# Kernel tuning notes

Measured on AMD Instinct MI355X. Metric: run time of the kernel, lower is better.

The kernel has to match this reference:

```python
import jax, jax.numpy as jnp
import numpy as np

B, T, D, H = 4, 1024, 2048, 16
E = D // H  # head_dim = 128


def setup_inputs() -> dict:
    key = jax.random.key(0)
    ks = jax.random.split(key, 10)
    s = 1.0 / np.sqrt(D)
    x = jax.random.normal(ks[0], (B, T, D), dtype=jnp.float32)
    attention_mask = jnp.ones((B, T), dtype=jnp.int32)
    # Per-head q/k/v projections stacked along head axis: [H, E, D] weights, [H, E] biases.
    Wq = jax.random.uniform(ks[1], (H, E, D), jnp.float32, -s, s)
    bq = jax.random.uniform(ks[2], (H, E), jnp.float32, -s, s)
    Wk = jax.random.uniform(ks[3], (H, E, D), jnp.float32, -s, s)
    bk = jax.random.uniform(ks[4], (H, E), jnp.float32, -s, s)
    Wv = jax.random.uniform(ks[5], (H, E, D), jnp.float32, -s, s)
    bv = jax.random.uniform(ks[6], (H, E), jnp.float32, -s, s)
    Wo = jax.random.uniform(ks[7], (D, D), jnp.float32, -s, s)
    bo = jax.random.uniform(ks[8], (D,), jnp.float32, -s, s)
    return {"x": x, "attention_mask": attention_mask, "Wq": Wq, "bq": bq,
            "Wk": Wk, "bk": bk, "Wv": Wv, "bv": bv, "Wo": Wo, "bo": bo}


def _causal_mask(Tq, Tk, dtype):
    neg = jnp.finfo(dtype).min
    qi = jnp.arange(Tq)[:, None]
    ki = jnp.arange(Tk)[None, :]
    max_allowed = Tk - Tq + qi
    return jnp.where(ki > max_allowed, neg, jnp.zeros((), dtype)).astype(dtype)


def reference(x, attention_mask, Wq, bq, Wk, bk, Wv, bv, Wo, bo):
    dt = x.dtype
    neg = jnp.finfo(dt).min
    scale = 1.0 / np.sqrt(E)
    # per-head projections (vectorized over heads): [B,H,T,E]
    q = jnp.einsum('btd,hed->bhte', x, Wq) + bq[None, :, None, :]
    k = jnp.einsum('btd,hed->bhte', x, Wk) + bk[None, :, None, :]
    v = jnp.einsum('btd,hed->bhte', x, Wv) + bv[None, :, None, :]
    # scores [B,H,Tq,Tk]
    scores = jnp.einsum('bhqe,bhke->bhqk', q, k) * scale
    scores = scores + _causal_mask(T, T, dt)[None, None]
    keep = attention_mask.astype(bool)  # [B,Tk]
    scores = jnp.where(keep[:, None, None, :], scores, neg)
    probs = jax.nn.softmax(scores, axis=-1)
    y = jnp.einsum('bhqk,bhke->bhqe', probs, v)  # [B,H,T,E]
    # heads concatenated along feature dim in head order
    y = jnp.transpose(y, (0, 2, 1, 3)).reshape(B, T, D)
    out = y @ Wo.T + bo
    return out
```

## Files before the change

### kernel.cpp

```cpp
#include <hip/hip_runtime.h>
#include <hip/hip_bf16.h>


typedef __attribute__((ext_vector_type(4))) float f32x4;
typedef __attribute__((ext_vector_type(8))) short s16x8;
typedef __attribute__((ext_vector_type(4))) unsigned short us16x4;

#define Td 1024
#define Dd 2048

__device__ __forceinline__ unsigned short f2bf(float f) {
  unsigned int u = __builtin_bit_cast(unsigned int, f);
  u = (u + 0x7fffu + ((u >> 16) & 1u)) >> 16;
  return (unsigned short)u;
}

__device__ __forceinline__ void gload_lds16(const void* g, void* l) {
  __builtin_amdgcn_global_load_lds(
      (const __attribute__((address_space(1))) unsigned int*)g,
      (__attribute__((address_space(3))) unsigned int*)l, 16, 0, 0);
}

__global__ void cvt_f32_bf16(const float* __restrict__ in,
                             unsigned short* __restrict__ out, int n4) {
  int i = blockIdx.x * 256 + threadIdx.x;
  if (i >= n4) return;
  float4 v = reinterpret_cast<const float4*>(in)[i];
  us16x4 o = {f2bf(v.x), f2bf(v.y), f2bf(v.z), f2bf(v.w)};
  reinterpret_cast<us16x4*>(out)[i] = o;
}

__global__ void bias_concat(const float* __restrict__ bq, const float* __restrict__ bk,
                            const float* __restrict__ bv, float* __restrict__ out) {
  int i = blockIdx.x * 256 + threadIdx.x;
  const float* s = (i < 2048) ? bq : ((i < 4096) ? bk : bv);
  out[i] = s[i & 2047];
}

template <int MODE>
__global__ __launch_bounds__(256, 2) void gemm_bt(
    const unsigned short* __restrict__ A, const unsigned short* __restrict__ Bm,
    const float* __restrict__ bias, void* __restrict__ C,
    unsigned short* __restrict__ Cv, int M, int N, int K, int ldc) {
  __shared__ unsigned short As[8192];
  __shared__ unsigned short Bs[8192];
  const int tid = threadIdx.x;
  const int lane = tid & 63, w = tid >> 6;
  const int g = lane >> 4, m15 = lane & 15;
  const int wr = w >> 1, wc = w & 1;
  const int row0 = blockIdx.y * 128, col0 = blockIdx.x * 128;

  f32x4 acc[4][4] = {};
  const int nK = K >> 6;
  for (int kt = 0; kt < nK; ++kt) {
    const int k0 = kt << 6;
    __syncthreads();
#pragma unroll
    for (int i = 0; i < 4; ++i) {
      const int p = w * 256 + i * 64 + lane;
      const int prow = p >> 3;
      const int lslot = (p & 7) ^ (prow & 7);
      gload_lds16(A + (size_t)(row0 + prow) * K + k0 + lslot * 8,
                  &As[(size_t)(w * 256 + i * 64) * 8]);
      gload_lds16(Bm + (size_t)(col0 + prow) * K + k0 + lslot * 8,
                  &Bs[(size_t)(w * 256 + i * 64) * 8]);
    }
    __syncthreads();
#pragma unroll
    for (int ks = 0; ks < 2; ++ks) {
      s16x8 af[4], bf[4];
#pragma unroll
      for (int i = 0; i < 4; ++i) {
        const int r = wr * 64 + i * 16 + m15;
        af[i] = *reinterpret_cast<const s16x8*>(&As[(r * 8 + ((ks * 4 + g) ^ (r & 7))) * 8]);
      }
#pragma unroll
      for (int j = 0; j < 4; ++j) {
        const int r = wc * 64 + j * 16 + m15;
        bf[j] = *reinterpret_cast<const s16x8*>(&Bs[(r * 8 + ((ks * 4 + g) ^ (r & 7))) * 8]);
      }
#pragma unroll
      for (int i = 0; i < 4; ++i)
#pragma unroll
        for (int j = 0; j < 4; ++j)
          acc[i][j] = __builtin_amdgcn_mfma_f32_16x16x32_bf16(af[i], bf[j], acc[i][j], 0, 0, 0);
    }
  }
  if (MODE == 1 && col0 >= 4096) {
    const int vc0 = col0 - 4096;
#pragma unroll
    for (int j = 0; j < 4; ++j) {
      const int vcol = vc0 + wc * 64 + j * 16 + m15;
      const float bv = bias[4096 + vcol];
      const int hh = vcol >> 7, e = vcol & 127;
#pragma unroll
      for (int i = 0; i < 4; ++i) {
        const int row = row0 + wr * 64 + i * 16 + g * 4;
        const int bb = row >> 10, tt = row & 1023;
        us16x4 pk;
#pragma unroll
        for (int r = 0; r < 4; ++r) pk[r] = f2bf(acc[i][j][r] + bv);
        *reinterpret_cast<us16x4*>(&Cv[((size_t)((bb * 16 + hh) * 128 + e)) * Td + tt]) = pk;
      }
    }
  } else {
#pragma unroll
    for (int j = 0; j < 4; ++j) {
      const int col = col0 + wc * 64 + j * 16 + m15;
      const float bv = bias[col];
#pragma unroll
      for (int i = 0; i < 4; ++i)
#pragma unroll
        for (int r = 0; r < 4; ++r) {
          const int row = row0 + wr * 64 + i * 16 + g * 4 + r;
          const float v = acc[i][j][r] + bv;
          if (MODE)
            ((unsigned short*)C)[(size_t)row * ldc + col] = f2bf(v);
          else
            ((float*)C)[(size_t)row * ldc + col] = v;
        }
    }
  }
}

#define SCALE 0.08838834764831845f

#define GRP_SOFTMAX(SF, G, QB)                                                 \
  {                                                                            \
    _Pragma("unroll") for (int kc = 0; kc < 4; ++kc) {                         \
      const int kgl = k0 + kc * 16 + m15;                                      \
      const int okm = am[kc];                                                  \
      _Pragma("unroll") for (int r = 0; r < 4; ++r) {                          \
        const int qg = (QB) + g * 4 + r;                                       \
        SF[kc][r] = (okm && kgl <= qg) ? SF[kc][r] * SCALE : -3.0e38f;         \
      }                                                                        \
    }                                                                          \
    _Pragma("unroll") for (int r = 0; r < 4; ++r) {                            \
      float t = fmaxf(fmaxf(SF[0][r], SF[1][r]), fmaxf(SF[2][r], SF[3][r]));   \
      t = fmaxf(t, __shfl_xor(t, 1));                                          \
      t = fmaxf(t, __shfl_xor(t, 2));                                          \
      t = fmaxf(t, __shfl_xor(t, 4));                                          \
      t = fmaxf(t, __shfl_xor(t, 8));                                          \
      const float mn = fmaxf(mrow[G][r], t);                                   \
      const float al = __expf(mrow[G][r] - mn);                                \
      mrow[G][r] = mn;                                                         \
      float rs = 0.f;                                                          \
      _Pragma("unroll") for (int kc = 0; kc < 4; ++kc) {                       \
        SF[kc][r] = __expf(SF[kc][r] - mn);                                    \
        rs += SF[kc][r];                                                       \
      }                                                                        \
      rs += __shfl_xor(rs, 1);                                                 \
      rs += __shfl_xor(rs, 2);                                                 \
      rs += __shfl_xor(rs, 4);                                                 \
      rs += __shfl_xor(rs, 8);                                                 \
      lrow[G][r] = lrow[G][r] * al + rs;                                       \
      _Pragma("unroll") for (int n = 0; n < 8; ++n) yacc[G][n][r] *= al;       \
    }                                                                          \
    _Pragma("unroll") for (int kc = 0; kc < 4; ++kc)                           \
        _Pragma("unroll") for (int r = 0; r < 4; ++r) {                        \
      const int prow = (G) * 16 + g * 4 + r;                                   \
      pw[prow * 64 + ((kc * 16 + m15) ^ ((prow & 7) << 3))] = f2bf(SF[kc][r]); \
    }                                                                          \
  }

__global__ __launch_bounds__(256, 2) void attn(
    const unsigned short* __restrict__ qk, const unsigned short* __restrict__ vt,
    const int* __restrict__ amask, unsigned short* __restrict__ Y) {
  __shared__ unsigned short Ks[2][8192];
  __shared__ unsigned short Vs[2][8192];
  __shared__ unsigned short Ps[4][2048];
  const int d = blockIdx.y * 8 + blockIdx.x;
  const int wk = (d & 7) * 64 + (d >> 3);
  const int p = wk & 7, bh = wk >> 3;
  const int b = bh >> 4, h = bh & 15;
  const int ta = p, tb = 15 - p;
  const int tid = threadIdx.x, lane = tid & 63, w = tid >> 6;
  const int g = lane >> 4, m15 = lane & 15;
  const int qab = ta * 64 + w * 16, qbb = tb * 64 + w * 16;
  unsigned short* pw = Ps[w];

  s16x8 qf[2][4];
#pragma unroll
  for (int G = 0; G < 2; ++G) {
    const int qb_ = G ? qbb : qab;
#pragma unroll
    for (int c = 0; c < 4; ++c)
      qf[G][c] = *reinterpret_cast<const s16x8*>(
          &qk[(size_t)(b * Td + qb_ + m15) * 4096 + h * 128 + c * 32 + g * 8]);
  }

  f32x4 yacc[2][8] = {};
  float mrow[2][4], lrow[2][4];
#pragma unroll
  for (int G = 0; G < 2; ++G)
#pragma unroll
    for (int r = 0; r < 4; ++r) { mrow[G][r] = -3.0e38f; lrow[G][r] = 0.f; }

  auto stage = [&](int buf, int kt) {
    const int k0s = kt << 6;
#pragma unroll
    for (int i = 0; i < 4; ++i) {
      const int pc = i * 256 + tid;
      const int krow = pc >> 4;
      const int ls = (pc & 15) ^ (krow & 7);
      gload_lds16(qk + (size_t)(b * Td + k0s + krow) * 4096 + 2048 + h * 128 + ls * 8,
                  &Ks[buf][(size_t)(i * 256 + w * 64) * 8]);
      const int e = pc >> 3;
      const int lv = (pc & 7) ^ (e & 7);
      gload_lds16(vt + (size_t)(bh * 128 + e) * Td + k0s + lv * 8,
                  &Vs[buf][(size_t)(i * 256 + w * 64) * 8]);
    }
  };

  const int nkt = tb + 1;
  stage(0, 0);
  asm volatile("s_waitcnt vmcnt(0)" ::: "memory");
  __syncthreads();
  int cur = 0;
  for (int kt = 0; kt < nkt; ++kt) {
    const int k0 = kt << 6;
    const bool actA = (kt <= ta);
    if (kt + 1 < nkt) stage(cur ^ 1, kt + 1);
    int am[4];
#pragma unroll
    for (int kc = 0; kc < 4; ++kc) am[kc] = amask[b * Td + k0 + kc * 16 + m15];

    f32x4 sf0[4] = {}, sf1[4] = {};
    __builtin_amdgcn_s_setprio(1);
#pragma unroll
    for (int kc = 0; kc < 4; ++kc) {
      const int krow = kc * 16 + m15;
#pragma unroll
      for (int c = 0; c < 4; ++c) {
        const s16x8 kf = *reinterpret_cast<const s16x8*>(
            &Ks[cur][(krow * 16 + ((c * 4 + g) ^ (krow & 7))) * 8]);
        if (actA) sf0[kc] = __builtin_amdgcn_mfma_f32_16x16x32_bf16(qf[0][c], kf, sf0[kc], 0, 0, 0);
        sf1[kc] = __builtin_amdgcn_mfma_f32_16x16x32_bf16(qf[1][c], kf, sf1[kc], 0, 0, 0);
      }
    }
    __builtin_amdgcn_s_setprio(0);

    if (actA) GRP_SOFTMAX(sf0, 0, qab)
    GRP_SOFTMAX(sf1, 1, qbb)

    asm volatile("s_waitcnt lgkmcnt(0)" ::: "memory");
    __builtin_amdgcn_sched_barrier(0);
    s16x8 pa0[2], pa1[2];
    if (actA) {
#pragma unroll
      for (int kcc = 0; kcc < 2; ++kcc)
        pa0[kcc] = *reinterpret_cast<const s16x8*>(
            &pw[m15 * 64 + ((kcc * 32 + g * 8) ^ ((m15 & 7) << 3))]);
    }
#pragma unroll
    for (int kcc = 0; kcc < 2; ++kcc) {
      const int prow = 16 + m15;
      pa1[kcc] = *reinterpret_cast<const s16x8*>(
          &pw[prow * 64 + ((kcc * 32 + g * 8) ^ ((prow & 7) << 3))]);
    }

    __builtin_amdgcn_s_setprio(1);
#pragma unroll
    for (int n = 0; n < 8; ++n) {
      const int e = n * 16 + m15;
#pragma unroll
      for (int kcc = 0; kcc < 2; ++kcc) {
        const s16x8 vf = *reinterpret_cast<const s16x8*>(
            &Vs[cur][(e * 8 + ((kcc * 4 + g) ^ (e & 7))) * 8]);
        if (actA) yacc[0][n] = __builtin_amdgcn_mfma_f32_16x16x32_bf16(pa0[kcc], vf, yacc[0][n], 0, 0, 0);
        yacc[1][n] = __builtin_amdgcn_mfma_f32_16x16x32_bf16(pa1[kcc], vf, yacc[1][n], 0, 0, 0);
      }
    }
    __builtin_amdgcn_s_setprio(0);

    asm volatile("s_waitcnt vmcnt(0)" ::: "memory");
    __syncthreads();
    cur ^= 1;
  }

#pragma unroll
  for (int G = 0; G < 2; ++G) {
    const int qb_ = G ? qbb : qab;
#pragma unroll
    for (int r = 0; r < 4; ++r) {
      const float inv = 1.0f / lrow[G][r];
      const size_t rowoff = (size_t)(b * Td + qb_ + g * 4 + r) * Dd + h * 128;
#pragma unroll
      for (int n = 0; n < 8; ++n)
        Y[rowoff + n * 16 + m15] = f2bf(yacc[G][n][r] * inv);
    }
  }
}

extern "C" void kernel_launch(void* const* d_in, const int* in_sizes, int n_in,
                              void* d_out, int out_size, void* d_ws, size_t ws_size,
                              hipStream_t stream) {
  const float* x = (const float*)d_in[0];
  const int* amask = (const int*)d_in[1];
  const float* Wq = (const float*)d_in[2];
  const float* bq = (const float*)d_in[3];
  const float* Wk = (const float*)d_in[4];
  const float* bk = (const float*)d_in[5];
  const float* Wv = (const float*)d_in[6];
  const float* bv = (const float*)d_in[7];
  const float* Wo = (const float*)d_in[8];
  const float* bo = (const float*)d_in[9];
  float* out = (float*)d_out;

  char* ws = (char*)d_ws;
  unsigned short* wqkv = (unsigned short*)(ws);
  unsigned short* xbf  = (unsigned short*)(ws + 25165824);
  unsigned short* qk   = (unsigned short*)(ws + 41943040);
  unsigned short* vt   = (unsigned short*)(ws + 75497472);
  unsigned short* wobf = (unsigned short*)(ws + 92274688);
  float* bqkv          = (float*)(ws + 100663296);
  unsigned short* ybuf = xbf;

  cvt_f32_bf16<<<8192, 256, 0, stream>>>(x, xbf, 2097152);
  cvt_f32_bf16<<<4096, 256, 0, stream>>>(Wq, wqkv, 1048576);
  cvt_f32_bf16<<<4096, 256, 0, stream>>>(Wk, wqkv + 4194304, 1048576);
  cvt_f32_bf16<<<4096, 256, 0, stream>>>(Wv, wqkv + 8388608, 1048576);
  cvt_f32_bf16<<<4096, 256, 0, stream>>>(Wo, wobf, 1048576);
  bias_concat<<<24, 256, 0, stream>>>(bq, bk, bv, bqkv);

  gemm_bt<1><<<dim3(48, 32), 256, 0, stream>>>(xbf, wqkv, bqkv, (void*)qk, vt, 4096, 6144, 2048, 4096);
  attn<<<dim3(8, 64), 256, 0, stream>>>(qk, vt, amask, ybuf);
  gemm_bt<0><<<dim3(16, 32), 256, 0, stream>>>(ybuf, wobf, bo, (void*)out, nullptr, 4096, 2048, 2048, 2048);
}
```

Measured before the change: 409.8 us.

## Restructure attention with transposed MFMA, smaller key tiles, bitmask and staged stores

The attention kernel now computes S^T by swapping the MFMA operands, so each lane owns one query row and softmax reductions need only two cross-lane shuffles. The key tile shrinks from 64 to 32, which halves LDS use and raises launch bounds to 3 blocks per CU. The attention mask is precomputed into per-batch bitmasks by a small new kernel, replacing per-tile integer loads. Output is staged through LDS so global writes are 16-byte vectors. The cost is twice as many loop iterations and barriers, plus an extra kernel launch.

```diff
diff --git a/kernel.cpp b/kernel.cpp
--- a/kernel.cpp
+++ b/kernel.cpp
@@ -5,9 +5,11 @@
 typedef __attribute__((ext_vector_type(4))) float f32x4;
 typedef __attribute__((ext_vector_type(8))) short s16x8;
 typedef __attribute__((ext_vector_type(4))) unsigned short us16x4;
+typedef __attribute__((ext_vector_type(8))) unsigned short us16x8;
 
 #define Td 1024
 #define Dd 2048
+#define SCALE 0.08838834764831845f
 
 __device__ __forceinline__ unsigned short f2bf(float f) {
   unsigned int u = __builtin_bit_cast(unsigned int, f);
@@ -35,6 +37,20 @@
   int i = blockIdx.x * 256 + threadIdx.x;
   const float* s = (i < 2048) ? bq : ((i < 4096) ? bk : bv);
   out[i] = s[i & 2047];
+}
+
+__global__ void prep_mask(const int* __restrict__ amask, unsigned* __restrict__ pmask) {
+  const int b = blockIdx.x, tid = threadIdx.x;
+  const int w = tid >> 6, lane = tid & 63;
+#pragma unroll
+  for (int j = 0; j < 4; ++j) {
+    const int k = j * 256 + tid;
+    unsigned long long ball = __ballot(amask[b * Td + k] != 0);
+    if (lane == 0) {
+      pmask[b * 32 + j * 8 + w * 2] = (unsigned)ball;
+      pmask[b * 32 + j * 8 + w * 2 + 1] = (unsigned)(ball >> 32);
+    }
+  }
 }
 
 template <int MODE>
@@ -123,52 +139,12 @@
   }
 }
 
-#define SCALE 0.08838834764831845f
-
-#define GRP_SOFTMAX(SF, G, QB)                                                 \
-  {                                                                            \
-    _Pragma("unroll") for (int kc = 0; kc < 4; ++kc) {                         \
-      const int kgl = k0 + kc * 16 + m15;                                      \
-      const int okm = am[kc];                                                  \
-      _Pragma("unroll") for (int r = 0; r < 4; ++r) {                          \
-        const int qg = (QB) + g * 4 + r;                                       \
-        SF[kc][r] = (okm && kgl <= qg) ? SF[kc][r] * SCALE : -3.0e38f;         \
-      }                                                                        \
-    }                                                                          \
-    _Pragma("unroll") for (int r = 0; r < 4; ++r) {                            \
-      float t = fmaxf(fmaxf(SF[0][r], SF[1][r]), fmaxf(SF[2][r], SF[3][r]));   \
-      t = fmaxf(t, __shfl_xor(t, 1));                                          \
-      t = fmaxf(t, __shfl_xor(t, 2));                                          \
-      t = fmaxf(t, __shfl_xor(t, 4));                                          \
-      t = fmaxf(t, __shfl_xor(t, 8));                                          \
-      const float mn = fmaxf(mrow[G][r], t);                                   \
-      const float al = __expf(mrow[G][r] - mn);                                \
-      mrow[G][r] = mn;                                                         \
-      float rs = 0.f;                                                          \
-      _Pragma("unroll") for (int kc = 0; kc < 4; ++kc) {                       \
-        SF[kc][r] = __expf(SF[kc][r] - mn);                                    \
-        rs += SF[kc][r];                                                       \
-      }                                                                        \
-      rs += __shfl_xor(rs, 1);                                                 \
-      rs += __shfl_xor(rs, 2);                                                 \
-      rs += __shfl_xor(rs, 4);                                                 \
-      rs += __shfl_xor(rs, 8);                                                 \
-      lrow[G][r] = lrow[G][r] * al + rs;                                       \
-      _Pragma("unroll") for (int n = 0; n < 8; ++n) yacc[G][n][r] *= al;       \
-    }                                                                          \
-    _Pragma("unroll") for (int kc = 0; kc < 4; ++kc)                           \
-        _Pragma("unroll") for (int r = 0; r < 4; ++r) {                        \
-      const int prow = (G) * 16 + g * 4 + r;                                   \
-      pw[prow * 64 + ((kc * 16 + m15) ^ ((prow & 7) << 3))] = f2bf(SF[kc][r]); \
-    }                                                                          \
-  }
-
-__global__ __launch_bounds__(256, 2) void attn(
+__global__ __launch_bounds__(256, 3) void attn(
     const unsigned short* __restrict__ qk, const unsigned short* __restrict__ vt,
-    const int* __restrict__ amask, unsigned short* __restrict__ Y) {
-  __shared__ unsigned short Ks[2][8192];
-  __shared__ unsigned short Vs[2][8192];
-  __shared__ unsigned short Ps[4][2048];
+    const unsigned* __restrict__ pmask, unsigned short* __restrict__ Y) {
+  __shared__ unsigned short Ks[2][4096];
+  __shared__ unsigned short Vs[2][4096];
+  __shared__ unsigned short Ps[4][1024];
   const int d = blockIdx.y * 8 + blockIdx.x;
   const int wk = (d & 7) * 64 + (d >> 3);
   const int p = wk & 7, bh = wk >> 3;
@@ -189,87 +165,108 @@
           &qk[(size_t)(b * Td + qb_ + m15) * 4096 + h * 128 + c * 32 + g * 8]);
   }
 
-  f32x4 yacc[2][8] = {};
-  float mrow[2][4], lrow[2][4];
-#pragma unroll
-  for (int G = 0; G < 2; ++G)
-#pragma unroll
-    for (int r = 0; r < 4; ++r) { mrow[G][r] = -3.0e38f; lrow[G][r] = 0.f; }
+  f32x4 yt[2][8] = {};
+  float m_[2] = {-3.0e38f, -3.0e38f}, l_[2] = {0.f, 0.f};
 
   auto stage = [&](int buf, int kt) {
-    const int k0s = kt << 6;
-#pragma unroll
-    for (int i = 0; i < 4; ++i) {
+    const int k0s = kt << 5;
+#pragma unroll
+    for (int i = 0; i < 2; ++i) {
       const int pc = i * 256 + tid;
-      const int krow = pc >> 4;
-      const int ls = (pc & 15) ^ (krow & 7);
-      gload_lds16(qk + (size_t)(b * Td + k0s + krow) * 4096 + 2048 + h * 128 + ls * 8,
-                  &Ks[buf][(size_t)(i * 256 + w * 64) * 8]);
-      const int e = pc >> 3;
-      const int lv = (pc & 7) ^ (e & 7);
-      gload_lds16(vt + (size_t)(bh * 128 + e) * Td + k0s + lv * 8,
-                  &Vs[buf][(size_t)(i * 256 + w * 64) * 8]);
+      const int kr = pc >> 4;
+      const int ls = (pc & 15) ^ (kr & 7);
+      gload_lds16(qk + (size_t)(b * Td + k0s + kr) * 4096 + 2048 + h * 128 + ls * 8,
+                  &Ks[buf][(i * 256 + w * 64) * 8]);
+      const int e = pc >> 2;
+      const int vs = (pc & 3) ^ (e & 3);
+      gload_lds16(vt + (size_t)(bh * 128 + e) * Td + k0s + vs * 8,
+                  &Vs[buf][(i * 256 + w * 64) * 8]);
     }
   };
 
-  const int nkt = tb + 1;
+  const int nkt = 2 * tb + 2;
   stage(0, 0);
   asm volatile("s_waitcnt vmcnt(0)" ::: "memory");
   __syncthreads();
   int cur = 0;
   for (int kt = 0; kt < nkt; ++kt) {
-    const int k0 = kt << 6;
-    const bool actA = (kt <= ta);
+    const int k0 = kt << 5;
+    const bool actA = (kt <= 2 * ta + 1);
     if (kt + 1 < nkt) stage(cur ^ 1, kt + 1);
-    int am[4];
-#pragma unroll
-    for (int kc = 0; kc < 4; ++kc) am[kc] = amask[b * Td + k0 + kc * 16 + m15];
-
-    f32x4 sf0[4] = {}, sf1[4] = {};
+    const unsigned pm = pmask[b * 32 + kt];
+
+    f32x4 s0[2] = {}, s1[2] = {};
     __builtin_amdgcn_s_setprio(1);
 #pragma unroll
-    for (int kc = 0; kc < 4; ++kc) {
+    for (int kc = 0; kc < 2; ++kc) {
       const int krow = kc * 16 + m15;
 #pragma unroll
       for (int c = 0; c < 4; ++c) {
         const s16x8 kf = *reinterpret_cast<const s16x8*>(
-            &Ks[cur][(krow * 16 + ((c * 4 + g) ^ (krow & 7))) * 8]);
-        if (actA) sf0[kc] = __builtin_amdgcn_mfma_f32_16x16x32_bf16(qf[0][c], kf, sf0[kc], 0, 0, 0);
-        sf1[kc] = __builtin_amdgcn_mfma_f32_16x16x32_bf16(qf[1][c], kf, sf1[kc], 0, 0, 0);
+            &Ks[cur][krow * 128 + (((c * 4 + g) ^ (krow & 7))) * 8]);
+        if (actA) s0[kc] = __builtin_amdgcn_mfma_f32_16x16x32_bf16(kf, qf[0][c], s0[kc], 0, 0, 0);
+        s1[kc] = __builtin_amdgcn_mfma_f32_16x16x32_bf16(kf, qf[1][c], s1[kc], 0, 0, 0);
       }
     }
     __builtin_amdgcn_s_setprio(0);
 
-    if (actA) GRP_SOFTMAX(sf0, 0, qab)
-    GRP_SOFTMAX(sf1, 1, qbb)
+    auto softmax_grp = [&](f32x4* s, int G, int qb_) {
+      const int q = qb_ + m15;
+      float pv[8];
+#pragma unroll
+      for (int kc = 0; kc < 2; ++kc)
+#pragma unroll
+        for (int r = 0; r < 4; ++r) {
+          const int bitp = kc * 16 + g * 4 + r;
+          const bool ok = ((pm >> bitp) & 1u) && (k0 + bitp <= q);
+          pv[kc * 4 + r] = ok ? s[kc][r] * SCALE : -3.0e38f;
+        }
+      float t = fmaxf(fmaxf(fmaxf(pv[0], pv[1]), fmaxf(pv[2], pv[3])),
+                      fmaxf(fmaxf(pv[4], pv[5]), fmaxf(pv[6], pv[7])));
+      t = fmaxf(t, __shfl_xor(t, 16));
+      t = fmaxf(t, __shfl_xor(t, 32));
+      const float mn = fmaxf(m_[G], t);
+      const float al = __expf(m_[G] - mn);
+      m_[G] = mn;
+      float rs = 0.f;
+#pragma unroll
+      for (int j = 0; j < 8; ++j) {
+        pv[j] = __expf(pv[j] - mn);
+        rs += pv[j];
+      }
+      rs += __shfl_xor(rs, 16);
+      rs += __shfl_xor(rs, 32);
+      l_[G] = l_[G] * al + rs;
+#pragma unroll
+      for (int n = 0; n < 8; ++n) yt[G][n] *= al;
+#pragma unroll
+      for (int kc = 0; kc < 2; ++kc) {
+        us16x4 pk;
+#pragma unroll
+        for (int r = 0; r < 4; ++r) pk[r] = f2bf(pv[kc * 4 + r]);
+        const int slot8 = kc * 4 + g;
+        const int idx = (G * 16 + m15) * 32 + (((slot8 >> 1) ^ (m15 & 3))) * 8 + (slot8 & 1) * 4;
+        *reinterpret_cast<us16x4*>(&pw[idx]) = pk;
+      }
+    };
+    if (actA) softmax_grp(s0, 0, qab);
+    softmax_grp(s1, 1, qbb);
 
     asm volatile("s_waitcnt lgkmcnt(0)" ::: "memory");
     __builtin_amdgcn_sched_barrier(0);
-    s16x8 pa0[2], pa1[2];
-    if (actA) {
-#pragma unroll
-      for (int kcc = 0; kcc < 2; ++kcc)
-        pa0[kcc] = *reinterpret_cast<const s16x8*>(
-            &pw[m15 * 64 + ((kcc * 32 + g * 8) ^ ((m15 & 7) << 3))]);
-    }
-#pragma unroll
-    for (int kcc = 0; kcc < 2; ++kcc) {
-      const int prow = 16 + m15;
-      pa1[kcc] = *reinterpret_cast<const s16x8*>(
-          &pw[prow * 64 + ((kcc * 32 + g * 8) ^ ((prow & 7) << 3))]);
-    }
+    s16x8 pf0, pf1;
+    if (actA)
+      pf0 = *reinterpret_cast<const s16x8*>(&pw[m15 * 32 + ((g ^ (m15 & 3))) * 8]);
+    pf1 = *reinterpret_cast<const s16x8*>(&pw[(16 + m15) * 32 + ((g ^ (m15 & 3))) * 8]);
 
     __builtin_amdgcn_s_setprio(1);
 #pragma unroll
-    for (int n = 0; n < 8; ++n) {
-      const int e = n * 16 + m15;
-#pragma unroll
-      for (int kcc = 0; kcc < 2; ++kcc) {
-        const s16x8 vf = *reinterpret_cast<const s16x8*>(
-            &Vs[cur][(e * 8 + ((kcc * 4 + g) ^ (e & 7))) * 8]);
-        if (actA) yacc[0][n] = __builtin_amdgcn_mfma_f32_16x16x32_bf16(pa0[kcc], vf, yacc[0][n], 0, 0, 0);
-        yacc[1][n] = __builtin_amdgcn_mfma_f32_16x16x32_bf16(pa1[kcc], vf, yacc[1][n], 0, 0, 0);
-      }
+    for (int nt = 0; nt < 8; ++nt) {
+      const int e = nt * 16 + m15;
+      const s16x8 vf = *reinterpret_cast<const s16x8*>(
+          &Vs[cur][e * 32 + ((g ^ (e & 3))) * 8]);
+      if (actA) yt[0][nt] = __builtin_amdgcn_mfma_f32_16x16x32_bf16(vf, pf0, yt[0][nt], 0, 0, 0);
+      yt[1][nt] = __builtin_amdgcn_mfma_f32_16x16x32_bf16(vf, pf1, yt[1][nt], 0, 0, 0);
     }
     __builtin_amdgcn_s_setprio(0);
 
@@ -281,13 +278,31 @@
 #pragma unroll
   for (int G = 0; G < 2; ++G) {
     const int qb_ = G ? qbb : qab;
-#pragma unroll
-    for (int r = 0; r < 4; ++r) {
-      const float inv = 1.0f / lrow[G][r];
-      const size_t rowoff = (size_t)(b * Td + qb_ + g * 4 + r) * Dd + h * 128;
-#pragma unroll
-      for (int n = 0; n < 8; ++n)
-        Y[rowoff + n * 16 + m15] = f2bf(yacc[G][n][r] * inv);
+    const float inv = 1.0f / l_[G];
+#pragma unroll
+    for (int half = 0; half < 2; ++half) {
+#pragma unroll
+      for (int ntl = 0; ntl < 4; ++ntl) {
+        const int nt = half * 4 + ntl;
+        us16x4 pk;
+#pragma unroll
+        for (int r = 0; r < 4; ++r) pk[r] = f2bf(yt[G][nt][r] * inv);
+        const int slot8 = ntl * 4 + g;
+        const int idx = m15 * 64 + (((slot8 >> 1) ^ (m15 & 7))) * 8 + (slot8 & 1) * 4;
+        *reinterpret_cast<us16x4*>(&pw[idx]) = pk;
+      }
+      asm volatile("s_waitcnt lgkmcnt(0)" ::: "memory");
+      __builtin_amdgcn_sched_barrier(0);
+      const int q = lane >> 2, c4 = lane & 3;
+#pragma unroll
+      for (int rr = 0; rr < 2; ++rr) {
+        const int pr = c4 + rr * 4;
+        us16x8 vv = *reinterpret_cast<const us16x8*>(&pw[q * 64 + ((pr ^ (q & 7))) * 8]);
+        *reinterpret_cast<us16x8*>(
+            &Y[(size_t)(b * Td + qb_ + q) * Dd + h * 128 + half * 64 + pr * 8]) = vv;
+      }
+      asm volatile("s_waitcnt lgkmcnt(0)" ::: "memory");
+      __builtin_amdgcn_sched_barrier(0);
     }
   }
 }
@@ -315,6 +330,7 @@
   unsigned short* wobf = (unsigned short*)(ws + 92274688);
   float* bqkv          = (float*)(ws + 100663296);
   unsigned short* ybuf = xbf;
+  unsigned* pmask      = (unsigned*)ws;
 
   cvt_f32_bf16<<<8192, 256, 0, stream>>>(x, xbf, 2097152);
   cvt_f32_bf16<<<4096, 256, 0, stream>>>(Wq, wqkv, 1048576);
@@ -324,6 +340,7 @@
   bias_concat<<<24, 256, 0, stream>>>(bq, bk, bv, bqkv);
 
   gemm_bt<1><<<dim3(48, 32), 256, 0, stream>>>(xbf, wqkv, bqkv, (void*)qk, vt, 4096, 6144, 2048, 4096);
-  attn<<<dim3(8, 64), 256, 0, stream>>>(qk, vt, amask, ybuf);
+  prep_mask<<<4, 256, 0, stream>>>(amask, pmask);
+  attn<<<dim3(8, 64), 256, 0, stream>>>(qk, vt, pmask, ybuf);
   gemm_bt<0><<<dim3(16, 32), 256, 0, stream>>>(ybuf, wobf, bo, (void*)out, nullptr, 4096, 2048, 2048, 2048);
 }
```

Result: slower. 488.0 us (+19.1%).
